# Kernel tuning notes

Hardware: AMD Instinct MI355X
Metric: run time of the kernel (lower is better)

Reference implementation:

```python
import jax, jax.numpy as jnp
import numpy as np

KK = 9  # 3x3 kernel points
PAD = 1
EPS = 1e-5


def _conv2d(x, w, b):
    # x: [B,C,H,W], w: [O,I,3,3]
    y = jax.lax.conv_general_dilated(
        x, w, window_strides=(1, 1), padding=((PAD, PAD), (PAD, PAD)),
        dimension_numbers=("NCHW", "OIHW", "NCHW"))
    return y + b[None, :, None, None]


def _bilinear_sample_one(img, py, px):
    # img: [C,H,W]; py, px: [KK,H,W] fractional sample coords
    C, H, W = img.shape
    y0 = jnp.floor(py).astype(jnp.int32)
    x0 = jnp.floor(px).astype(jnp.int32)
    wy = py - y0
    wx = px - x0

    def g(yi, xi):
        ok = ((yi >= 0) & (yi < H) & (xi >= 0) & (xi < W)).astype(img.dtype)
        v = img[:, jnp.clip(yi, 0, H - 1), jnp.clip(xi, 0, W - 1)]  # [C,KK,H,W]
        return v * ok[None]

    v00 = g(y0, x0)
    v01 = g(y0, x0 + 1)
    v10 = g(y0 + 1, x0)
    v11 = g(y0 + 1, x0 + 1)
    return (v00 * (1 - wy) * (1 - wx) + v01 * (1 - wy) * wx
            + v10 * wy * (1 - wx) + v11 * wy * wx)  # [C,KK,H,W]


def setup_inputs() -> dict:
    key = jax.random.key(0)
    ks = jax.random.split(key, 8)
    B, C, H, W = 8, 256, 96, 96
    O = 256
    x = jax.random.normal(ks[0], (B, C, H, W), dtype=jnp.float32)
    # modulated DCNv2 offset/mask conv: 3*KK output channels
    w_off = jax.random.normal(ks[1], (3 * KK, C, 3, 3), dtype=jnp.float32) * 0.01
    b_off = jnp.zeros((3 * KK,), dtype=jnp.float32)
    w_dcn = jax.random.normal(ks[2], (O, C, 3, 3), dtype=jnp.float32) * (1.0 / np.sqrt(C * KK))
    b_dcn = jnp.zeros((O,), dtype=jnp.float32)
    gamma = jnp.ones((O,), dtype=jnp.float32)
    beta = jnp.zeros((O,), dtype=jnp.float32)
    running_mean = jax.random.normal(ks[3], (O,), dtype=jnp.float32) * 0.1
    running_var = jax.random.uniform(ks[4], (O,), dtype=jnp.float32, minval=0.5, maxval=1.5)
    return {"x": x, "w_off": w_off, "b_off": b_off, "w_dcn": w_dcn,
            "b_dcn": b_dcn, "gamma": gamma, "beta": beta,
            "running_mean": running_mean, "running_var": running_var}


def reference(x, w_off, b_off, w_dcn, b_dcn, gamma, beta, running_mean, running_var):
    B, C, H, W = x.shape
    O = w_dcn.shape[0]
    # offsets + modulation masks
    om = _conv2d(x, w_off, b_off)                  # [B, 3*KK, H, W]
    offset = om[:, :2 * KK]
    mask = jax.nn.sigmoid(om[:, 2 * KK:])          # [B, KK, H, W]
    off_y = offset[:, 0::2]                        # [B, KK, H, W]
    off_x = offset[:, 1::2]

    ky, kx = jnp.meshgrid(jnp.arange(3), jnp.arange(3), indexing="ij")
    ky = ky.reshape(KK).astype(x.dtype)
    kx = kx.reshape(KK).astype(x.dtype)
    hh = jnp.arange(H, dtype=x.dtype)
    ww = jnp.arange(W, dtype=x.dtype)
    # fractional sampling coordinates per output pixel per kernel point
    py = off_y + hh[None, None, :, None] + ky[None, :, None, None] - PAD
    px = off_x + ww[None, None, None, :] + kx[None, :, None, None] - PAD

    sampled = jax.vmap(_bilinear_sample_one)(x, py, px)  # [B,C,KK,H,W]
    sampled = sampled * mask[:, None]
    out = jnp.einsum("bckhw,ock->bohw", sampled, w_dcn.reshape(O, C, KK))
    out = out + b_dcn[None, :, None, None]
    # BatchNorm (inference, running stats) + ReLU
    inv = jax.lax.rsqrt(running_var + EPS)
    out = (out - running_mean[None, :, None, None]) * (gamma * inv)[None, :, None, None]
    out = out + beta[None, :, None, None]
    return jax.nn.relu(out)
```

## Files before the change

### kernel.cpp

```cpp
#include <hip/hip_runtime.h>
#include <hip/hip_bf16.h>
#include <cstdint>
#include <cstddef>

#define H 96
#define W 96
#define HW 9216
#define C 256
#define B 8
#define O 256
#define KK 9
#define EPS 1e-5f

typedef __attribute__((ext_vector_type(8))) short short8;
typedef __attribute__((ext_vector_type(4))) float float4v;
typedef unsigned short ushort_t;
typedef unsigned int uint_t;

__global__ __launch_bounds__(256) void transpose_x_k(
    const float* __restrict__ x, ushort_t* __restrict__ xt)
{
    __shared__ float tile[64][65];
    int t = threadIdx.x;
    int p0 = blockIdx.x * 64;
    int c0 = blockIdx.y * 64;
    int b  = blockIdx.z;
    {
        int tx = t & 63, ty = t >> 6;
        const float* xb = x + ((size_t)b * C + c0 + ty) * HW + p0 + tx;
#pragma unroll
        for (int i = 0; i < 64; i += 4)
            tile[ty + i][tx] = xb[(size_t)i * HW];
    }
    __syncthreads();
    {
        int tc = t & 31, tp = t >> 5;
        ushort_t* xtb = xt + ((size_t)b * HW + p0) * C + c0;
#pragma unroll
        for (int i = 0; i < 64; i += 8) {
            int p = tp + i;
            float a  = tile[2 * tc][p];
            float bb = tile[2 * tc + 1][p];
            __hip_bfloat162 h2 = __float22bfloat162_rn(make_float2(a, bb));
            uint_t u;
            __builtin_memcpy(&u, &h2, 4);
            *reinterpret_cast<uint_t*>(&xtb[(size_t)p * C + 2 * tc]) = u;
        }
    }
}

__global__ __launch_bounds__(256) void prep_b_k(
    const float* __restrict__ wd, ushort_t* __restrict__ bp)
{
    int idx = blockIdx.x * 256 + threadIdx.x;
    int kk = idx / (O * C);
    int r = idx - kk * O * C;
    int o = r >> 8, c = r & 255;
    float v = wd[((size_t)o * C + c) * KK + kk];
    __hip_bfloat16 hh = __float2bfloat16(v);
    ushort_t u;
    __builtin_memcpy(&u, &hh, 2);
    bp[idx] = u;
}

__global__ __launch_bounds__(256) void prep_bo_k(
    const float* __restrict__ wo, ushort_t* __restrict__ bo)
{
    int idx = blockIdx.x * 256 + threadIdx.x;
    int n = idx / (KK * C);
    int r = idx - n * KK * C;
    int kk = r >> 8, c = r & 255;
    float v = (n < 27) ? wo[((size_t)n * C + c) * KK + kk] : 0.0f;
    __hip_bfloat16 hh = __float2bfloat16(v);
    ushort_t u;
    __builtin_memcpy(&u, &hh, 2);
    bo[idx] = u;
}

__global__ __launch_bounds__(256) void offset_mfma_k(
    const ushort_t* __restrict__ xt, const ushort_t* __restrict__ bo,
    const float* __restrict__ b_off, float* __restrict__ om)
{
    int t = threadIdx.x;
    int wv = t >> 6, l = t & 63;
    int ln = l & 15, lq = l >> 4;
    int p0 = blockIdx.x * 128;
    int b = p0 / HW;
    int rem0w = p0 - b * HW + wv * 32;
    const ushort_t* xtb = xt + (size_t)b * HW * C;

    int hh0[2], ww0[2];
#pragma unroll
    for (int mt = 0; mt < 2; ++mt) {
        int rem = rem0w + mt * 16 + ln;
        hh0[mt] = rem / W;
        ww0[mt] = rem - hh0[mt] * W;
    }

    float4v acc[2][2];
#pragma unroll
    for (int i = 0; i < 2; ++i)
#pragma unroll
        for (int j = 0; j < 2; ++j) acc[i][j] = (float4v){0.f, 0.f, 0.f, 0.f};

#pragma unroll
    for (int kk = 0; kk < KK; ++kk) {
        int dy = kk / 3 - 1, dx = kk % 3 - 1;
        const ushort_t* ap[2];
        bool okv[2];
#pragma unroll
        for (int mt = 0; mt < 2; ++mt) {
            int hh = hh0[mt] + dy, ww = ww0[mt] + dx;
            okv[mt] = (hh >= 0) & (hh < H) & (ww >= 0) & (ww < W);
            ap[mt] = xtb + (size_t)(hh * W + ww) * C + lq * 8;
        }
        const ushort_t* bp0 = bo + ((size_t)(0 * 16 + ln) * KK + kk) * C + lq * 8;
        const ushort_t* bp1 = bo + ((size_t)(1 * 16 + ln) * KK + kk) * C + lq * 8;
#pragma unroll
        for (int cc = 0; cc < 8; ++cc) {
            int c0 = cc * 32;
            short8 af[2];
#pragma unroll
            for (int mt = 0; mt < 2; ++mt) {
                short8 v = (short8)0;
                if (okv[mt]) v = *(const short8*)(ap[mt] + c0);
                af[mt] = v;
            }
            short8 bf0 = *(const short8*)(bp0 + c0);
            short8 bf1 = *(const short8*)(bp1 + c0);
#pragma unroll
            for (int mt = 0; mt < 2; ++mt) {
                acc[mt][0] = __builtin_amdgcn_mfma_f32_16x16x32_bf16(af[mt], bf0, acc[mt][0], 0, 0, 0);
                acc[mt][1] = __builtin_amdgcn_mfma_f32_16x16x32_bf16(af[mt], bf1, acc[mt][1], 0, 0, 0);
            }
        }
    }

    float* omb = om + (size_t)b * 27 * HW + rem0w;
#pragma unroll
    for (int nt = 0; nt < 2; ++nt) {
        int oc = nt * 16 + ln;
        if (oc < 27) {
            float bv = b_off[oc];
            float* po = omb + (size_t)oc * HW + lq * 4;
#pragma unroll
            for (int mt = 0; mt < 2; ++mt) {
                float4 v;
                v.x = acc[mt][nt].x + bv;
                v.y = acc[mt][nt].y + bv;
                v.z = acc[mt][nt].z + bv;
                v.w = acc[mt][nt].w + bv;
                *(float4*)(po + mt * 16) = v;
            }
        }
    }
}

__device__ __forceinline__ void unpack8(uint4 q, float* v) {
    v[0] = __uint_as_float(q.x << 16);
    v[1] = __uint_as_float(q.x & 0xffff0000u);
    v[2] = __uint_as_float(q.y << 16);
    v[3] = __uint_as_float(q.y & 0xffff0000u);
    v[4] = __uint_as_float(q.z << 16);
    v[5] = __uint_as_float(q.z & 0xffff0000u);
    v[6] = __uint_as_float(q.w << 16);
    v[7] = __uint_as_float(q.w & 0xffff0000u);
}

__device__ __forceinline__ uint_t packbf2(float a, float b) {
    __hip_bfloat162 h2 = __float22bfloat162_rn(make_float2(a, b));
    uint_t u;
    __builtin_memcpy(&u, &h2, 4);
    return u;
}

__global__ __launch_bounds__(256) void dcn_main_k(
    const ushort_t* __restrict__ xt, const float* __restrict__ om,
    const ushort_t* __restrict__ bp, const float* __restrict__ b_dcn,
    const float* __restrict__ gamma, const float* __restrict__ beta,
    const float* __restrict__ rmean, const float* __restrict__ rvar,
    float* __restrict__ out)
{
    __shared__ uint4    s_rec[64 * KK][2];
    __shared__ ushort_t s_a[2][64][40];

    int t = threadIdx.x;
    int p0 = blockIdx.x * 64;
    int b = p0 / HW;
    int rem0 = p0 - b * HW;

    for (int v = t; v < 64 * KK; v += 256) {
        int m = v / KK;
        int k = v - m * KK;
        int rem = rem0 + m;
        int h = rem / W;
        int w = rem - h * W;
        const float* omb = om + (size_t)b * 27 * HW + rem;
        float offy = omb[(size_t)(2 * k) * HW];
        float offx = omb[(size_t)(2 * k + 1) * HW];
        float z    = omb[(size_t)(18 + k) * HW];
        float mval = 1.0f / (1.0f + __expf(-z));
        float py = (float)(h + k / 3 - 1) + offy;
        float px = (float)(w + k % 3 - 1) + offx;
        float fy = floorf(py), fx = floorf(px);
        int y0 = (int)fy, x0 = (int)fx;
        float wy = py - fy, wx = px - fx;
        float row0f = (1.0f - wy) * mval * ((y0 >= 0 && y0 < H) ? 1.0f : 0.0f);
        float row1f = wy * mval * ((y0 >= -1 && y0 < H - 1) ? 1.0f : 0.0f);
        int xsel = min(max(x0, 0), W - 2);
        float wxa = (x0 >= 0 && x0 < W) ? (1.0f - wx) : 0.0f;
        float wxb = (x0 >= -1 && x0 < W - 1) ? wx : 0.0f;
        int cx0 = min(max(x0, 0), W - 1);
        int cx1 = min(max(x0 + 1, 0), W - 1);
        float wA = ((cx0 == xsel) ? wxa : 0.0f) + ((cx1 == xsel) ? wxb : 0.0f);
        float wB = ((cx0 == xsel + 1) ? wxa : 0.0f) + ((cx1 == xsel + 1) ? wxb : 0.0f);
        int yc0 = min(max(y0, 0), H - 1);
        int yc1 = min(max(y0 + 1, 0), H - 1);
        uint4 r0, r1;
        r0.x = (uint_t)((yc0 * W + xsel) * C);
        r0.y = (uint_t)((yc1 * W + xsel) * C);
        r0.z = __float_as_uint(row0f * wA);
        r0.w = __float_as_uint(row0f * wB);
        r1.x = __float_as_uint(row1f * wA);
        r1.y = __float_as_uint(row1f * wB);
        r1.z = 0; r1.w = 0;
        s_rec[v][0] = r0;
        s_rec[v][1] = r1;
    }

    float4v acc[4][4];
#pragma unroll
    for (int i = 0; i < 4; ++i)
#pragma unroll
        for (int j = 0; j < 4; ++j)
            acc[i][j] = (float4v){0.f, 0.f, 0.f, 0.f};

    const ushort_t* xtb = xt + (size_t)b * HW * C;
    int wv = t >> 6;
    int l  = t & 63;
    int ln = l & 15;
    int lq = l >> 4;
    int sm = t >> 2;
    int sc = (t & 3) * 8;

    __syncthreads();

    int buf = 0;
    for (int kk = 0; kk < KK; ++kk) {
        uint4 r0 = s_rec[sm * KK + kk][0];
        uint4 r1 = s_rec[sm * KK + kk][1];
        const ushort_t* pr0 = xtb + r0.x + sc;
        const ushort_t* pr1 = xtb + r0.y + sc;
        float wA0 = __uint_as_float(r0.z), wB0 = __uint_as_float(r0.w);
        float wA1 = __uint_as_float(r1.x), wB1 = __uint_as_float(r1.y);
        const ushort_t* bpk = bp + (size_t)kk * O * C + (size_t)(wv * 64 + ln) * C + lq * 8;

        for (int ci = 0; ci < 8; ++ci) {
            int c0 = ci * 32;
            uint4 q00 = *(const uint4*)(pr0 + c0);
            uint4 q01 = *(const uint4*)(pr0 + c0 + C);
            uint4 q10 = *(const uint4*)(pr1 + c0);
            uint4 q11 = *(const uint4*)(pr1 + c0 + C);
            short8 bfr[4];
#pragma unroll
            for (int nt = 0; nt < 4; ++nt)
                bfr[nt] = *(const short8*)(bpk + (size_t)(nt * 16) * C + c0);

            float v00[8], v01[8], v10[8], v11[8], val[8];
            unpack8(q00, v00); unpack8(q01, v01);
            unpack8(q10, v10); unpack8(q11, v11);
#pragma unroll
            for (int j = 0; j < 8; ++j)
                val[j] = v00[j] * wA0 + v01[j] * wB0 + v10[j] * wA1 + v11[j] * wB1;
            uint4 pk;
            pk.x = packbf2(val[0], val[1]);
            pk.y = packbf2(val[2], val[3]);
            pk.z = packbf2(val[4], val[5]);
            pk.w = packbf2(val[6], val[7]);
            *(uint4*)&s_a[buf][sm][sc] = pk;

            __syncthreads();

            short8 af[4];
#pragma unroll
            for (int mt = 0; mt < 4; ++mt)
                af[mt] = *(const short8*)&s_a[buf][mt * 16 + ln][lq * 8];
#pragma unroll
            for (int mt = 0; mt < 4; ++mt)
#pragma unroll
                for (int nt = 0; nt < 4; ++nt)
                    acc[mt][nt] = __builtin_amdgcn_mfma_f32_16x16x32_bf16(
                        af[mt], bfr[nt], acc[mt][nt], 0, 0, 0);
            buf ^= 1;
        }
    }

#pragma unroll
    for (int nt = 0; nt < 4; ++nt) {
        int o = wv * 64 + nt * 16 + ln;
        float scale = gamma[o] * rsqrtf(rvar[o] + EPS);
        float shift = (b_dcn[o] - rmean[o]) * scale + beta[o];
        float* po = out + ((size_t)b * O + o) * HW + rem0 + lq * 4;
#pragma unroll
        for (int mt = 0; mt < 4; ++mt) {
            float4 vv;
            vv.x = fmaxf(acc[mt][nt].x * scale + shift, 0.0f);
            vv.y = fmaxf(acc[mt][nt].y * scale + shift, 0.0f);
            vv.z = fmaxf(acc[mt][nt].z * scale + shift, 0.0f);
            vv.w = fmaxf(acc[mt][nt].w * scale + shift, 0.0f);
            *(float4*)(po + mt * 16) = vv;
        }
    }
}

extern "C" void kernel_launch(void* const* d_in, const int* in_sizes, int n_in,
                              void* d_out, int out_size, void* d_ws, size_t ws_size,
                              hipStream_t stream) {
    const float* x     = (const float*)d_in[0];
    const float* w_off = (const float*)d_in[1];
    const float* b_off = (const float*)d_in[2];
    const float* w_dcn = (const float*)d_in[3];
    const float* b_dcn = (const float*)d_in[4];
    const float* gamma = (const float*)d_in[5];
    const float* beta  = (const float*)d_in[6];
    const float* rmean = (const float*)d_in[7];
    const float* rvar  = (const float*)d_in[8];
    float* out = (float*)d_out;

    float*    om  = (float*)d_ws;
    ushort_t* bpw = (ushort_t*)(om + (size_t)B * 27 * HW);
    ushort_t* bow = bpw + (size_t)KK * O * C;
    ushort_t* xtw = bow + (size_t)32 * KK * C;

    hipLaunchKernelGGL(transpose_x_k, dim3(144, 4, 8), dim3(256), 0, stream,
                       x, xtw);
    hipLaunchKernelGGL(prep_b_k, dim3(2304), dim3(256), 0, stream,
                       w_dcn, bpw);
    hipLaunchKernelGGL(prep_bo_k, dim3(288), dim3(256), 0, stream,
                       w_off, bow);
    hipLaunchKernelGGL(offset_mfma_k, dim3(73728 / 128), dim3(256), 0, stream,
                       xtw, bow, b_off, om);
    hipLaunchKernelGGL(dcn_main_k, dim3(73728 / 64), dim3(256), 0, stream,
                       xtw, om, bpw, b_dcn, gamma, beta, rmean, rvar, out);
}
```

Measured before the change: 502.7 us.

## Prefetch next gather slice in registers and halve barriers in DCN main kernel

Restructures the DCN main loop so each thread owns one output pixel and 16 channels, and each iteration covers 64 channels instead of 32. The bilinear corner loads for the next iteration are issued into registers before the current slice is written to LDS, overlapping global gather latency with the MFMA work and halving the number of barriers. Sampling records are split into SoA arrays with kernel-point-major indexing, and both the offset and main kernels remap block indices across the 8 batches to spread work across XCDs/caches. Register pressure rises because of the prefetch buffer, and the LDS layout for A tiles loses its padding, which may cause bank conflicts.

```diff
diff --git a/kernel.cpp b/kernel.cpp
--- a/kernel.cpp
+++ b/kernel.cpp
@@ -84,7 +84,9 @@
     int t = threadIdx.x;
     int wv = t >> 6, l = t & 63;
     int ln = l & 15, lq = l >> 4;
-    int p0 = blockIdx.x * 128;
+    int d = blockIdx.x;
+    int lb = (d & 7) * 72 + (d >> 3);
+    int p0 = lb * 128;
     int b = p0 / HW;
     int rem0w = p0 - b * HW + wv * 32;
     const ushort_t* xtb = xt + (size_t)b * HW * C;
@@ -181,17 +183,20 @@
     const float* __restrict__ rmean, const float* __restrict__ rvar,
     float* __restrict__ out)
 {
-    __shared__ uint4    s_rec[64 * KK][2];
-    __shared__ ushort_t s_a[2][64][40];
+    __shared__ uint4    s_rec0[64 * KK];
+    __shared__ float2   s_rec1[64 * KK];
+    __shared__ ushort_t s_a[2][2][64][32];
 
     int t = threadIdx.x;
-    int p0 = blockIdx.x * 64;
+    int d = blockIdx.x;
+    int lb = (d & 7) * 144 + (d >> 3);
+    int p0 = lb * 64;
     int b = p0 / HW;
     int rem0 = p0 - b * HW;
 
     for (int v = t; v < 64 * KK; v += 256) {
-        int m = v / KK;
-        int k = v - m * KK;
+        int m = v & 63;
+        int k = v >> 6;
         int rem = rem0 + m;
         int h = rem / W;
         int w = rem - h * W;
@@ -216,16 +221,13 @@
         float wB = ((cx0 == xsel + 1) ? wxa : 0.0f) + ((cx1 == xsel + 1) ? wxb : 0.0f);
         int yc0 = min(max(y0, 0), H - 1);
         int yc1 = min(max(y0 + 1, 0), H - 1);
-        uint4 r0, r1;
+        uint4 r0;
         r0.x = (uint_t)((yc0 * W + xsel) * C);
         r0.y = (uint_t)((yc1 * W + xsel) * C);
         r0.z = __float_as_uint(row0f * wA);
         r0.w = __float_as_uint(row0f * wB);
-        r1.x = __float_as_uint(row1f * wA);
-        r1.y = __float_as_uint(row1f * wB);
-        r1.z = 0; r1.w = 0;
-        s_rec[v][0] = r0;
-        s_rec[v][1] = r1;
+        s_rec0[v] = r0;
+        s_rec1[v] = make_float2(row1f * wA, row1f * wB);
     }
 
     float4v acc[4][4];
@@ -240,58 +242,87 @@
     int l  = t & 63;
     int ln = l & 15;
     int lq = l >> 4;
-    int sm = t >> 2;
-    int sc = (t & 3) * 8;
+    int m  = t & 63;
+    int g  = t >> 6;
+    int coff = g * 8;
 
     __syncthreads();
 
-    int buf = 0;
-    for (int kk = 0; kk < KK; ++kk) {
-        uint4 r0 = s_rec[sm * KK + kk][0];
-        uint4 r1 = s_rec[sm * KK + kk][1];
-        const ushort_t* pr0 = xtb + r0.x + sc;
-        const ushort_t* pr1 = xtb + r0.y + sc;
-        float wA0 = __uint_as_float(r0.z), wB0 = __uint_as_float(r0.w);
-        float wA1 = __uint_as_float(r1.x), wB1 = __uint_as_float(r1.y);
-        const ushort_t* bpk = bp + (size_t)kk * O * C + (size_t)(wv * 64 + ln) * C + lq * 8;
-
-        for (int ci = 0; ci < 8; ++ci) {
-            int c0 = ci * 32;
-            uint4 q00 = *(const uint4*)(pr0 + c0);
-            uint4 q01 = *(const uint4*)(pr0 + c0 + C);
-            uint4 q10 = *(const uint4*)(pr1 + c0);
-            uint4 q11 = *(const uint4*)(pr1 + c0 + C);
-            short8 bfr[4];
+    uint4 L[8];
+    float Wt[4];
+    {
+        uint4 r0 = s_rec0[m];
+        float2 r1 = s_rec1[m];
+        const ushort_t* q0 = xtb + r0.x + coff;
+        const ushort_t* q1 = xtb + r0.y + coff;
+        Wt[0] = __uint_as_float(r0.z); Wt[1] = __uint_as_float(r0.w);
+        Wt[2] = r1.x; Wt[3] = r1.y;
+#pragma unroll
+        for (int j = 0; j < 2; ++j) {
+            L[j * 4 + 0] = *(const uint4*)(q0 + j * 32);
+            L[j * 4 + 1] = *(const uint4*)(q0 + C + j * 32);
+            L[j * 4 + 2] = *(const uint4*)(q1 + j * 32);
+            L[j * 4 + 3] = *(const uint4*)(q1 + C + j * 32);
+        }
+    }
+
+    for (int it = 0; it < 36; ++it) {
+        int kk = it >> 2, q = it & 3;
+        int buf = it & 1;
+
+        uint4 pk[2];
+#pragma unroll
+        for (int j = 0; j < 2; ++j) {
+            float v0[8], v1[8], v2[8], v3[8], val[8];
+            unpack8(L[j * 4 + 0], v0); unpack8(L[j * 4 + 1], v1);
+            unpack8(L[j * 4 + 2], v2); unpack8(L[j * 4 + 3], v3);
+#pragma unroll
+            for (int e = 0; e < 8; ++e)
+                val[e] = v0[e] * Wt[0] + v1[e] * Wt[1] + v2[e] * Wt[2] + v3[e] * Wt[3];
+            pk[j].x = packbf2(val[0], val[1]);
+            pk[j].y = packbf2(val[2], val[3]);
+            pk[j].z = packbf2(val[4], val[5]);
+            pk[j].w = packbf2(val[6], val[7]);
+        }
+
+        int nit = it + 1;
+        if (nit < 36) {
+            int nkk = nit >> 2, nq = nit & 3;
+            uint4 r0 = s_rec0[nkk * 64 + m];
+            float2 r1 = s_rec1[nkk * 64 + m];
+            const ushort_t* q0 = xtb + r0.x + nq * 64 + coff;
+            const ushort_t* q1 = xtb + r0.y + nq * 64 + coff;
+            Wt[0] = __uint_as_float(r0.z); Wt[1] = __uint_as_float(r0.w);
+            Wt[2] = r1.x; Wt[3] = r1.y;
+#pragma unroll
+            for (int j = 0; j < 2; ++j) {
+                L[j * 4 + 0] = *(const uint4*)(q0 + j * 32);
+                L[j * 4 + 1] = *(const uint4*)(q0 + C + j * 32);
+                L[j * 4 + 2] = *(const uint4*)(q1 + j * 32);
+                L[j * 4 + 3] = *(const uint4*)(q1 + C + j * 32);
+            }
+        }
+
+        *(uint4*)&s_a[buf][0][m][coff] = pk[0];
+        *(uint4*)&s_a[buf][1][m][coff] = pk[1];
+        __syncthreads();
+
+#pragma unroll
+        for (int j = 0; j < 2; ++j) {
+            short8 bfr[4], af[4];
 #pragma unroll
             for (int nt = 0; nt < 4; ++nt)
-                bfr[nt] = *(const short8*)(bpk + (size_t)(nt * 16) * C + c0);
-
-            float v00[8], v01[8], v10[8], v11[8], val[8];
-            unpack8(q00, v00); unpack8(q01, v01);
-            unpack8(q10, v10); unpack8(q11, v11);
-#pragma unroll
-            for (int j = 0; j < 8; ++j)
-                val[j] = v00[j] * wA0 + v01[j] * wB0 + v10[j] * wA1 + v11[j] * wB1;
-            uint4 pk;
-            pk.x = packbf2(val[0], val[1]);
-            pk.y = packbf2(val[2], val[3]);
-            pk.z = packbf2(val[4], val[5]);
-            pk.w = packbf2(val[6], val[7]);
-            *(uint4*)&s_a[buf][sm][sc] = pk;
-
-            __syncthreads();
-
-            short8 af[4];
+                bfr[nt] = *(const short8*)(bp + ((size_t)kk * O + wv * 64 + nt * 16 + ln) * C
+                                           + q * 64 + j * 32 + lq * 8);
 #pragma unroll
             for (int mt = 0; mt < 4; ++mt)
-                af[mt] = *(const short8*)&s_a[buf][mt * 16 + ln][lq * 8];
+                af[mt] = *(const short8*)&s_a[buf][j][mt * 16 + ln][lq * 8];
 #pragma unroll
             for (int mt = 0; mt < 4; ++mt)
 #pragma unroll
                 for (int nt = 0; nt < 4; ++nt)
                     acc[mt][nt] = __builtin_amdgcn_mfma_f32_16x16x32_bf16(
                         af[mt], bfr[nt], acc[mt][nt], 0, 0, 0);
-            buf ^= 1;
         }
     }
 
```

Measured after the change: 572.4 us. 13.9% more time.
